# Optimization experiments

Hardware: AMD Instinct MI355X
Metric: run time of the kernel (lower is better)

## Reference

```python
import jax, jax.numpy as jnp
import numpy as np

N_IN = 64
N_HID = 128


def setup_inputs() -> dict:
    key = jax.random.key(0)
    k_x, k_wih, k_bih, k_whh, k_bhh = jax.random.split(key, 5)
    S, B = 1024, 4096
    x = jax.random.normal(k_x, (S, B, N_IN), dtype=jnp.float32)
    # torch.nn.Linear weights: W [out, in], b [out]
    lim_ih = 1.0 / np.sqrt(N_IN)
    lim_hh = 1.0 / np.sqrt(N_HID)
    W_ih = jax.random.uniform(k_wih, (N_HID, N_IN), jnp.float32, -lim_ih, lim_ih)
    b_ih = jax.random.uniform(k_bih, (N_HID,), jnp.float32, -lim_ih, lim_ih)
    W_hh = jax.random.uniform(k_whh, (N_HID, N_HID), jnp.float32, -lim_hh, lim_hh)
    b_hh = jax.random.uniform(k_bhh, (N_HID,), jnp.float32, -lim_hh, lim_hh)
    return {"x": x, "W_ih": W_ih, "b_ih": b_ih, "W_hh": W_hh, "b_hh": b_hh}


def reference(x, W_ih, b_ih, W_hh, b_hh):
    # Elman RNN: h_t = tanh(x_t @ W_ih^T + b_ih + h_{t-1} @ W_hh^T + b_hh)
    # x: [S, B, 64]; returns final hidden state [B, 128]
    B = x.shape[1]
    h0 = jnp.zeros((B, N_HID), dtype=x.dtype)
    # Precompute the input projection for all timesteps (one big GEMM).
    xp = jnp.einsum('sbi,hi->sbh', x, W_ih) + b_ih  # [S, B, 128]

    def step(h, xp_t):
        h_new = jnp.tanh(xp_t + h @ W_hh.T + b_hh)
        return h_new, None

    h_final, _ = jax.lax.scan(step, h0, xp)
    return h_final
```

## Files before the change

kernel.cpp:

```cpp
#include <hip/hip_runtime.h>

#define S_LEN 1024
#define BATCH 4096
#define NIN 64
#define NHID 128
#define BT 16

typedef __attribute__((ext_vector_type(8))) short bf16x8;
typedef __attribute__((ext_vector_type(4))) float f32x4;

__device__ __forceinline__ unsigned cvt_pk(float lo, float hi) {
    unsigned r;
    asm("v_cvt_pk_bf16_f32 %0, %1, %2" : "=v"(r) : "v"(lo), "v"(hi));
    return r;
}
__device__ __forceinline__ float tanh_fast(float z) {
    float u = __builtin_amdgcn_exp2f(z * 2.885390081777927f);
    return (u - 1.0f) * __builtin_amdgcn_rcpf(u + 1.0f);
}
__device__ __forceinline__ void lds_barrier() {
    asm volatile("s_waitcnt lgkmcnt(0)\n\ts_barrier" ::: "memory");
    __builtin_amdgcn_sched_barrier(0);
}

#define MFMA __builtin_amdgcn_mfma_f32_16x16x32_bf16


__global__ __launch_bounds__(256, 1)
void rnn_kernel(const float* __restrict__ x,
                const float* __restrict__ W_ih,
                const float* __restrict__ b_ih,
                const float* __restrict__ W_hh,
                const float* __restrict__ b_hh,
                float* __restrict__ out)
{
    __shared__ __align__(16) char lds[8192];
    const int tid  = threadIdx.x;
    const int wv   = tid >> 6;
    const int lane = tid & 63;
    const int col  = lane & 15;
    const int kg   = lane >> 4;
    const int bb0  = blockIdx.x * BT;

    for (int i = tid; i < 2048; i += 256) ((int*)lds)[i] = 0;

    const int OWN = wv;
    char* lbx = lds + (lane << 4);
    char*       wp  = lbx + (OWN << 10);
    const char* rp1 = lbx + ((((OWN + 1) & 3)) << 10);
    const char* rp2 = lbx + ((((OWN + 2) & 3)) << 10);
    const char* rp3 = lbx + ((((OWN + 3) & 3)) << 10);

    bf16x8 whh0[4], whh1[4];
    const int tt0 = 2 * OWN, tt1 = tt0 + 1;
    #pragma unroll
    for (int q = 0; q < 4; ++q) {
        const int kkq = (OWN + q) & 3;
        {
            const float* pw = W_hh + (16 * tt0 + col) * NHID + 32 * kkq + 4 * kg;
            f32x4 c0 = *(const f32x4*)(pw);
            f32x4 c1 = *(const f32x4*)(pw + 16);
            union { bf16x8 v; unsigned u[4]; } fr;
            fr.u[0] = cvt_pk(c0[0], c0[1]); fr.u[1] = cvt_pk(c0[2], c0[3]);
            fr.u[2] = cvt_pk(c1[0], c1[1]); fr.u[3] = cvt_pk(c1[2], c1[3]);
            whh0[q] = fr.v;
        }
        {
            const float* pw = W_hh + (16 * tt1 + col) * NHID + 32 * kkq + 4 * kg;
            f32x4 c0 = *(const f32x4*)(pw);
            f32x4 c1 = *(const f32x4*)(pw + 16);
            union { bf16x8 v; unsigned u[4]; } fr;
            fr.u[0] = cvt_pk(c0[0], c0[1]); fr.u[1] = cvt_pk(c0[2], c0[3]);
            fr.u[2] = cvt_pk(c1[0], c1[1]); fr.u[3] = cvt_pk(c1[2], c1[3]);
            whh1[q] = fr.v;
        }
    }
    bf16x8 wihA0, wihB0, wihA1, wihB1;
    {
        const float* q0 = W_ih + (16 * tt0 + col) * NIN + 8 * kg;
        const float* q1 = W_ih + (16 * tt1 + col) * NIN + 8 * kg;
        union { bf16x8 v; unsigned u[4]; } fr;
        f32x4 c0, c1;
        c0 = *(const f32x4*)(q0);      c1 = *(const f32x4*)(q0 + 4);
        fr.u[0] = cvt_pk(c0[0], c0[1]); fr.u[1] = cvt_pk(c0[2], c0[3]);
        fr.u[2] = cvt_pk(c1[0], c1[1]); fr.u[3] = cvt_pk(c1[2], c1[3]);
        wihA0 = fr.v;
        c0 = *(const f32x4*)(q0 + 32); c1 = *(const f32x4*)(q0 + 36);
        fr.u[0] = cvt_pk(c0[0], c0[1]); fr.u[1] = cvt_pk(c0[2], c0[3]);
        fr.u[2] = cvt_pk(c1[0], c1[1]); fr.u[3] = cvt_pk(c1[2], c1[3]);
        wihB0 = fr.v;
        c0 = *(const f32x4*)(q1);      c1 = *(const f32x4*)(q1 + 4);
        fr.u[0] = cvt_pk(c0[0], c0[1]); fr.u[1] = cvt_pk(c0[2], c0[3]);
        fr.u[2] = cvt_pk(c1[0], c1[1]); fr.u[3] = cvt_pk(c1[2], c1[3]);
        wihA1 = fr.v;
        c0 = *(const f32x4*)(q1 + 32); c1 = *(const f32x4*)(q1 + 36);
        fr.u[0] = cvt_pk(c0[0], c0[1]); fr.u[1] = cvt_pk(c0[2], c0[3]);
        fr.u[2] = cvt_pk(c1[0], c1[1]); fr.u[3] = cvt_pk(c1[2], c1[3]);
        wihB1 = fr.v;
    }
    f32x4 bias0, bias1;
    {
        f32x4 bi = *(const f32x4*)(b_ih + 16 * tt0 + 4 * kg);
        f32x4 bh = *(const f32x4*)(b_hh + 16 * tt0 + 4 * kg);
        bias0 = bi + bh;
        bi = *(const f32x4*)(b_ih + 16 * tt1 + 4 * kg);
        bh = *(const f32x4*)(b_hh + 16 * tt1 + 4 * kg);
        bias1 = bi + bh;
    }

    const float* xlane = x + ((size_t)bb0 + col) * NIN + kg * 8;

    auto loadStage = [&](f32x4& v0, f32x4& v1, f32x4& v2, f32x4& v3, int t) {
        if (t < S_LEN) {
            const float* p = xlane + (size_t)t * (BATCH * NIN);
            v0 = *(const f32x4*)(p);      v1 = *(const f32x4*)(p + 4);
            v2 = *(const f32x4*)(p + 32); v3 = *(const f32x4*)(p + 36);
        }
    };
    auto computeXP = [&](const f32x4& v0, const f32x4& v1,
                         const f32x4& v2, const f32x4& v3,
                         f32x4& o0, f32x4& o1) {
        union { bf16x8 v; unsigned u[4]; } xa, xb;
        xa.u[0] = cvt_pk(v0[0], v0[1]); xa.u[1] = cvt_pk(v0[2], v0[3]);
        xa.u[2] = cvt_pk(v1[0], v1[1]); xa.u[3] = cvt_pk(v1[2], v1[3]);
        xb.u[0] = cvt_pk(v2[0], v2[1]); xb.u[1] = cvt_pk(v2[2], v2[3]);
        xb.u[2] = cvt_pk(v3[0], v3[1]); xb.u[3] = cvt_pk(v3[2], v3[3]);
        f32x4 p0 = bias0, p1 = bias1;
        p0 = MFMA(wihA0, xa.v, p0, 0, 0, 0);
        p1 = MFMA(wihA1, xa.v, p1, 0, 0, 0);
        p0 = MFMA(wihB0, xb.v, p0, 0, 0, 0);
        p1 = MFMA(wihB1, xb.v, p1, 0, 0, 0);
        o0 = p0; o1 = p1;
    };

    f32x4 S00, S01, S02, S03, S10, S11, S12, S13;
    f32x4 S20, S21, S22, S23, S30, S31, S32, S33;
    loadStage(S00, S01, S02, S03, 0);
    loadStage(S10, S11, S12, S13, 1);
    loadStage(S20, S21, S22, S23, 2);
    loadStage(S30, S31, S32, S33, 3);
    f32x4 xc0, xc1, xn0, xn1;
    computeXP(S00, S01, S02, S03, xc0, xc1);
    loadStage(S00, S01, S02, S03, 4);
    bf16x8 Bo = {0, 0, 0, 0, 0, 0, 0, 0};
    __syncthreads();

    auto cstep = [&](int t, f32x4& s0, f32x4& s1, f32x4& s2, f32x4& s3,
                     const f32x4& c0, const f32x4& c1,
                     f32x4& n0, f32x4& n1, bool last) {
        const int rb = (t & 1) << 12;
        bf16x8 P1 = *(const bf16x8*)(rp1 + rb);
        bf16x8 P2 = *(const bf16x8*)(rp2 + rb);
        bf16x8 P3 = *(const bf16x8*)(rp3 + rb);

        f32x4 a0 = c0, a1 = c1;
        a0 = MFMA(whh0[0], Bo, a0, 0, 0, 0);
        a1 = MFMA(whh1[0], Bo, a1, 0, 0, 0);

        computeXP(s0, s1, s2, s3, n0, n1);
        loadStage(s0, s1, s2, s3, t + 5);

        a0 = MFMA(whh0[1], P1, a0, 0, 0, 0);
        a1 = MFMA(whh1[1], P1, a1, 0, 0, 0);
        a0 = MFMA(whh0[2], P2, a0, 0, 0, 0);
        a1 = MFMA(whh1[2], P2, a1, 0, 0, 0);
        a0 = MFMA(whh0[3], P3, a0, 0, 0, 0);
        a1 = MFMA(whh1[3], P3, a1, 0, 0, 0);

        #pragma unroll
        for (int i = 0; i < 4; ++i) a0[i] = tanh_fast(a0[i]);
        #pragma unroll
        for (int i = 0; i < 4; ++i) a1[i] = tanh_fast(a1[i]);

        if (last) {
            float* ob = out + ((size_t)bb0 + col) * NHID + 32 * OWN + 4 * kg;
            *(f32x4*)(ob)      = a0;
            *(f32x4*)(ob + 16) = a1;
        } else {
            union { bf16x8 v; unsigned u[4]; } fb;
            fb.u[0] = cvt_pk(a0[0], a0[1]); fb.u[1] = cvt_pk(a0[2], a0[3]);
            fb.u[2] = cvt_pk(a1[0], a1[1]); fb.u[3] = cvt_pk(a1[2], a1[3]);
            Bo = fb.v;
            *(bf16x8*)(wp + (((t + 1) & 1) << 12)) = Bo;
        }
        lds_barrier();
    };

    for (int m = 0; m < 255; ++m) {
        const int t = 4 * m;
        cstep(t + 0, S10, S11, S12, S13, xc0, xc1, xn0, xn1, false);
        cstep(t + 1, S20, S21, S22, S23, xn0, xn1, xc0, xc1, false);
        cstep(t + 2, S30, S31, S32, S33, xc0, xc1, xn0, xn1, false);
        cstep(t + 3, S00, S01, S02, S03, xn0, xn1, xc0, xc1, false);
    }
    cstep(1020, S10, S11, S12, S13, xc0, xc1, xn0, xn1, false);
    cstep(1021, S20, S21, S22, S23, xn0, xn1, xc0, xc1, false);
    cstep(1022, S30, S31, S32, S33, xc0, xc1, xn0, xn1, false);
    cstep(1023, S00, S01, S02, S03, xn0, xn1, xc0, xc1, true);
}

extern "C" void kernel_launch(void* const* d_in, const int* in_sizes, int n_in,
                              void* d_out, int out_size, void* d_ws, size_t ws_size,
                              hipStream_t stream) {
    const float* x    = (const float*)d_in[0];
    const float* W_ih = (const float*)d_in[1];
    const float* b_ih = (const float*)d_in[2];
    const float* W_hh = (const float*)d_in[3];
    const float* b_hh = (const float*)d_in[4];
    float* out = (float*)d_out;

    dim3 grid(BATCH / BT);
    dim3 block(256);
    rnn_kernel<<<grid, block, 0, stream>>>(x, W_ih, b_ih, W_hh, b_hh, out);
}
```

Measured before the change: 455.5 us.

## Exchange partial W_hh products through LDS instead of hidden-state fragments

Restructures the recurrent step so each wave multiplies its own hidden slice by every output tile's W_hh block and writes fp32 partial sums to LDS. After the barrier, the owner wave sums the partials and applies tanh, which takes the MFMA chain off the critical path between barriers. The cost is eight times more LDS traffic (64 KB buffer, 6 float4 writes and reads per step) and a shallower x prefetch. tanh is also rewritten as 1 - 2/(u+1).

New measurement: 548.9 us. 20.5% more time.

```diff
diff --git a/kernel.cpp b/kernel.cpp
--- a/kernel.cpp
+++ b/kernel.cpp
@@ -16,7 +16,7 @@
 }
 __device__ __forceinline__ float tanh_fast(float z) {
     float u = __builtin_amdgcn_exp2f(z * 2.885390081777927f);
-    return (u - 1.0f) * __builtin_amdgcn_rcpf(u + 1.0f);
+    return fmaf(-2.0f, __builtin_amdgcn_rcpf(u + 1.0f), 1.0f);
 }
 __device__ __forceinline__ void lds_barrier() {
     asm volatile("s_waitcnt lgkmcnt(0)\n\ts_barrier" ::: "memory");
@@ -24,6 +24,13 @@
 }
 
 #define MFMA __builtin_amdgcn_mfma_f32_16x16x32_bf16
+
+__device__ __forceinline__ bf16x8 pack8(const f32x4& a, const f32x4& b) {
+    union { bf16x8 v; unsigned u[4]; } r;
+    r.u[0] = cvt_pk(a[0], a[1]); r.u[1] = cvt_pk(a[2], a[3]);
+    r.u[2] = cvt_pk(b[0], b[1]); r.u[3] = cvt_pk(b[2], b[3]);
+    return r.v;
+}
 
 
 __global__ __launch_bounds__(256, 1)
@@ -34,7 +41,7 @@
                 const float* __restrict__ b_hh,
                 float* __restrict__ out)
 {
-    __shared__ __align__(16) char lds[8192];
+    __shared__ __align__(16) char lds[65536];
     const int tid  = threadIdx.x;
     const int wv   = tid >> 6;
     const int lane = tid & 63;
@@ -42,61 +49,44 @@
     const int kg   = lane >> 4;
     const int bb0  = blockIdx.x * BT;
 
-    for (int i = tid; i < 2048; i += 256) ((int*)lds)[i] = 0;
+    for (int i = tid; i < 16384; i += 256) ((int*)lds)[i] = 0;
 
     const int OWN = wv;
+    const int o1 = (OWN + 1) & 3, o2 = (OWN + 2) & 3, o3 = (OWN + 3) & 3;
     char* lbx = lds + (lane << 4);
-    char*       wp  = lbx + (OWN << 10);
-    const char* rp1 = lbx + ((((OWN + 1) & 3)) << 10);
-    const char* rp2 = lbx + ((((OWN + 2) & 3)) << 10);
-    const char* rp3 = lbx + ((((OWN + 3) & 3)) << 10);
-
-    bf16x8 whh0[4], whh1[4];
+    char* w10 = lbx + ((o1 * 8 + OWN * 2 + 0) << 10);
+    char* w11 = lbx + ((o1 * 8 + OWN * 2 + 1) << 10);
+    char* w20 = lbx + ((o2 * 8 + OWN * 2 + 0) << 10);
+    char* w21 = lbx + ((o2 * 8 + OWN * 2 + 1) << 10);
+    char* w30 = lbx + ((o3 * 8 + OWN * 2 + 0) << 10);
+    char* w31 = lbx + ((o3 * 8 + OWN * 2 + 1) << 10);
+    const char* r10 = lbx + ((OWN * 8 + o1 * 2 + 0) << 10);
+    const char* r11 = lbx + ((OWN * 8 + o1 * 2 + 1) << 10);
+    const char* r20 = lbx + ((OWN * 8 + o2 * 2 + 0) << 10);
+    const char* r21 = lbx + ((OWN * 8 + o2 * 2 + 1) << 10);
+    const char* r30 = lbx + ((OWN * 8 + o3 * 2 + 0) << 10);
+    const char* r31 = lbx + ((OWN * 8 + o3 * 2 + 1) << 10);
+
+    auto loadWhh = [&](int nt) -> bf16x8 {
+        const float* pw = W_hh + (size_t)(16 * nt + col) * NHID + 32 * OWN + 4 * kg;
+        f32x4 c0 = *(const f32x4*)(pw);
+        f32x4 c1 = *(const f32x4*)(pw + 16);
+        return pack8(c0, c1);
+    };
+    bf16x8 whhP10 = loadWhh(2 * o1),  whhP11 = loadWhh(2 * o1 + 1);
+    bf16x8 whhP20 = loadWhh(2 * o2),  whhP21 = loadWhh(2 * o2 + 1);
+    bf16x8 whhP30 = loadWhh(2 * o3),  whhP31 = loadWhh(2 * o3 + 1);
+    bf16x8 whhO0  = loadWhh(2 * OWN), whhO1  = loadWhh(2 * OWN + 1);
+
     const int tt0 = 2 * OWN, tt1 = tt0 + 1;
-    #pragma unroll
-    for (int q = 0; q < 4; ++q) {
-        const int kkq = (OWN + q) & 3;
-        {
-            const float* pw = W_hh + (16 * tt0 + col) * NHID + 32 * kkq + 4 * kg;
-            f32x4 c0 = *(const f32x4*)(pw);
-            f32x4 c1 = *(const f32x4*)(pw + 16);
-            union { bf16x8 v; unsigned u[4]; } fr;
-            fr.u[0] = cvt_pk(c0[0], c0[1]); fr.u[1] = cvt_pk(c0[2], c0[3]);
-            fr.u[2] = cvt_pk(c1[0], c1[1]); fr.u[3] = cvt_pk(c1[2], c1[3]);
-            whh0[q] = fr.v;
-        }
-        {
-            const float* pw = W_hh + (16 * tt1 + col) * NHID + 32 * kkq + 4 * kg;
-            f32x4 c0 = *(const f32x4*)(pw);
-            f32x4 c1 = *(const f32x4*)(pw + 16);
-            union { bf16x8 v; unsigned u[4]; } fr;
-            fr.u[0] = cvt_pk(c0[0], c0[1]); fr.u[1] = cvt_pk(c0[2], c0[3]);
-            fr.u[2] = cvt_pk(c1[0], c1[1]); fr.u[3] = cvt_pk(c1[2], c1[3]);
-            whh1[q] = fr.v;
-        }
-    }
     bf16x8 wihA0, wihB0, wihA1, wihB1;
     {
-        const float* q0 = W_ih + (16 * tt0 + col) * NIN + 8 * kg;
-        const float* q1 = W_ih + (16 * tt1 + col) * NIN + 8 * kg;
-        union { bf16x8 v; unsigned u[4]; } fr;
-        f32x4 c0, c1;
-        c0 = *(const f32x4*)(q0);      c1 = *(const f32x4*)(q0 + 4);
-        fr.u[0] = cvt_pk(c0[0], c0[1]); fr.u[1] = cvt_pk(c0[2], c0[3]);
-        fr.u[2] = cvt_pk(c1[0], c1[1]); fr.u[3] = cvt_pk(c1[2], c1[3]);
-        wihA0 = fr.v;
-        c0 = *(const f32x4*)(q0 + 32); c1 = *(const f32x4*)(q0 + 36);
-        fr.u[0] = cvt_pk(c0[0], c0[1]); fr.u[1] = cvt_pk(c0[2], c0[3]);
-        fr.u[2] = cvt_pk(c1[0], c1[1]); fr.u[3] = cvt_pk(c1[2], c1[3]);
-        wihB0 = fr.v;
-        c0 = *(const f32x4*)(q1);      c1 = *(const f32x4*)(q1 + 4);
-        fr.u[0] = cvt_pk(c0[0], c0[1]); fr.u[1] = cvt_pk(c0[2], c0[3]);
-        fr.u[2] = cvt_pk(c1[0], c1[1]); fr.u[3] = cvt_pk(c1[2], c1[3]);
-        wihA1 = fr.v;
-        c0 = *(const f32x4*)(q1 + 32); c1 = *(const f32x4*)(q1 + 36);
-        fr.u[0] = cvt_pk(c0[0], c0[1]); fr.u[1] = cvt_pk(c0[2], c0[3]);
-        fr.u[2] = cvt_pk(c1[0], c1[1]); fr.u[3] = cvt_pk(c1[2], c1[3]);
-        wihB1 = fr.v;
+        const float* q0 = W_ih + (size_t)(16 * tt0 + col) * NIN + 8 * kg;
+        const float* q1 = W_ih + (size_t)(16 * tt1 + col) * NIN + 8 * kg;
+        wihA0 = pack8(*(const f32x4*)(q0),      *(const f32x4*)(q0 + 4));
+        wihB0 = pack8(*(const f32x4*)(q0 + 32), *(const f32x4*)(q0 + 36));
+        wihA1 = pack8(*(const f32x4*)(q1),      *(const f32x4*)(q1 + 4));
+        wihB1 = pack8(*(const f32x4*)(q1 + 32), *(const f32x4*)(q1 + 36));
     }
     f32x4 bias0, bias1;
     {
@@ -109,7 +99,6 @@
     }
 
     const float* xlane = x + ((size_t)bb0 + col) * NIN + kg * 8;
-
     auto loadStage = [&](f32x4& v0, f32x4& v1, f32x4& v2, f32x4& v3, int t) {
         if (t < S_LEN) {
             const float* p = xlane + (size_t)t * (BATCH * NIN);
@@ -117,86 +106,90 @@
             v2 = *(const f32x4*)(p + 32); v3 = *(const f32x4*)(p + 36);
         }
     };
-    auto computeXP = [&](const f32x4& v0, const f32x4& v1,
-                         const f32x4& v2, const f32x4& v3,
-                         f32x4& o0, f32x4& o1) {
-        union { bf16x8 v; unsigned u[4]; } xa, xb;
-        xa.u[0] = cvt_pk(v0[0], v0[1]); xa.u[1] = cvt_pk(v0[2], v0[3]);
-        xa.u[2] = cvt_pk(v1[0], v1[1]); xa.u[3] = cvt_pk(v1[2], v1[3]);
-        xb.u[0] = cvt_pk(v2[0], v2[1]); xb.u[1] = cvt_pk(v2[2], v2[3]);
-        xb.u[2] = cvt_pk(v3[0], v3[1]); xb.u[3] = cvt_pk(v3[2], v3[3]);
+    auto computeXP = [&](const bf16x8& xa, const bf16x8& xb,
+                         f32x4& q0, f32x4& q1) {
         f32x4 p0 = bias0, p1 = bias1;
-        p0 = MFMA(wihA0, xa.v, p0, 0, 0, 0);
-        p1 = MFMA(wihA1, xa.v, p1, 0, 0, 0);
-        p0 = MFMA(wihB0, xb.v, p0, 0, 0, 0);
-        p1 = MFMA(wihB1, xb.v, p1, 0, 0, 0);
-        o0 = p0; o1 = p1;
-    };
-
-    f32x4 S00, S01, S02, S03, S10, S11, S12, S13;
-    f32x4 S20, S21, S22, S23, S30, S31, S32, S33;
-    loadStage(S00, S01, S02, S03, 0);
-    loadStage(S10, S11, S12, S13, 1);
-    loadStage(S20, S21, S22, S23, 2);
-    loadStage(S30, S31, S32, S33, 3);
-    f32x4 xc0, xc1, xn0, xn1;
-    computeXP(S00, S01, S02, S03, xc0, xc1);
-    loadStage(S00, S01, S02, S03, 4);
-    bf16x8 Bo = {0, 0, 0, 0, 0, 0, 0, 0};
+        p0 = MFMA(wihA0, xa, p0, 0, 0, 0);
+        p1 = MFMA(wihA1, xa, p1, 0, 0, 0);
+        p0 = MFMA(wihB0, xb, p0, 0, 0, 0);
+        p1 = MFMA(wihB1, xb, p1, 0, 0, 0);
+        q0 = p0; q1 = p1;
+    };
+
+    f32x4 A0, A1, A2, A3, B0, B1, B2, B3;
+    bf16x8 PCa, PCb, PNa, PNb;
+    f32x4 pO0, pO1;
+    loadStage(A0, A1, A2, A3, 0);
+    PCa = pack8(A0, A1); PCb = pack8(A2, A3);
+    computeXP(PCa, PCb, pO0, pO1);
+    loadStage(A0, A1, A2, A3, 1);
+    PCa = pack8(A0, A1); PCb = pack8(A2, A3);
+    loadStage(A0, A1, A2, A3, 2);
+    loadStage(B0, B1, B2, B3, 3);
     __syncthreads();
 
     auto cstep = [&](int t, f32x4& s0, f32x4& s1, f32x4& s2, f32x4& s3,
-                     const f32x4& c0, const f32x4& c1,
-                     f32x4& n0, f32x4& n1, bool last) {
-        const int rb = (t & 1) << 12;
-        bf16x8 P1 = *(const bf16x8*)(rp1 + rb);
-        bf16x8 P2 = *(const bf16x8*)(rp2 + rb);
-        bf16x8 P3 = *(const bf16x8*)(rp3 + rb);
-
-        f32x4 a0 = c0, a1 = c1;
-        a0 = MFMA(whh0[0], Bo, a0, 0, 0, 0);
-        a1 = MFMA(whh1[0], Bo, a1, 0, 0, 0);
-
-        computeXP(s0, s1, s2, s3, n0, n1);
-        loadStage(s0, s1, s2, s3, t + 5);
-
-        a0 = MFMA(whh0[1], P1, a0, 0, 0, 0);
-        a1 = MFMA(whh1[1], P1, a1, 0, 0, 0);
-        a0 = MFMA(whh0[2], P2, a0, 0, 0, 0);
-        a1 = MFMA(whh1[2], P2, a1, 0, 0, 0);
-        a0 = MFMA(whh0[3], P3, a0, 0, 0, 0);
-        a1 = MFMA(whh1[3], P3, a1, 0, 0, 0);
-
+                     const bf16x8& pca, const bf16x8& pcb,
+                     bf16x8& pna, bf16x8& pnb, bool last) {
+        const int rb = (t & 1) << 15;
+        f32x4 q10 = *(const f32x4*)(r10 + rb);
+        f32x4 q11 = *(const f32x4*)(r11 + rb);
+        f32x4 q20 = *(const f32x4*)(r20 + rb);
+        f32x4 q21 = *(const f32x4*)(r21 + rb);
+        f32x4 q30 = *(const f32x4*)(r30 + rb);
+        f32x4 q31 = *(const f32x4*)(r31 + rb);
+        f32x4 xq0, xq1;
+        if (t + 1 < S_LEN) computeXP(pca, pcb, xq0, xq1);
+        f32x4 pre0 = (pO0 + q10) + (q20 + q30);
+        f32x4 pre1 = (pO1 + q11) + (q21 + q31);
+        f32x4 v0, v1;
         #pragma unroll
-        for (int i = 0; i < 4; ++i) a0[i] = tanh_fast(a0[i]);
+        for (int i = 0; i < 4; ++i) v0[i] = tanh_fast(pre0[i]);
         #pragma unroll
-        for (int i = 0; i < 4; ++i) a1[i] = tanh_fast(a1[i]);
+        for (int i = 0; i < 4; ++i) v1[i] = tanh_fast(pre1[i]);
 
         if (last) {
             float* ob = out + ((size_t)bb0 + col) * NHID + 32 * OWN + 4 * kg;
-            *(f32x4*)(ob)      = a0;
-            *(f32x4*)(ob + 16) = a1;
-        } else {
+            *(f32x4*)(ob)      = v0;
+            *(f32x4*)(ob + 16) = v1;
+            lds_barrier();
+            return;
+        }
+        bf16x8 Bo;
+        {
             union { bf16x8 v; unsigned u[4]; } fb;
-            fb.u[0] = cvt_pk(a0[0], a0[1]); fb.u[1] = cvt_pk(a0[2], a0[3]);
-            fb.u[2] = cvt_pk(a1[0], a1[1]); fb.u[3] = cvt_pk(a1[2], a1[3]);
+            fb.u[0] = cvt_pk(v0[0], v0[1]); fb.u[1] = cvt_pk(v0[2], v0[3]);
+            fb.u[2] = cvt_pk(v1[0], v1[1]); fb.u[3] = cvt_pk(v1[2], v1[3]);
             Bo = fb.v;
-            *(bf16x8*)(wp + (((t + 1) & 1) << 12)) = Bo;
         }
+        const int nb = ((t + 1) & 1) << 15;
+        const f32x4 z4 = {0.f, 0.f, 0.f, 0.f};
+        f32x4 g10 = MFMA(whhP10, Bo, z4, 0, 0, 0);
+        f32x4 g11 = MFMA(whhP11, Bo, z4, 0, 0, 0);
+        f32x4 g20 = MFMA(whhP20, Bo, z4, 0, 0, 0);
+        f32x4 g21 = MFMA(whhP21, Bo, z4, 0, 0, 0);
+        f32x4 g30 = MFMA(whhP30, Bo, z4, 0, 0, 0);
+        f32x4 g31 = MFMA(whhP31, Bo, z4, 0, 0, 0);
+        *(f32x4*)(w10 + nb) = g10;
+        *(f32x4*)(w11 + nb) = g11;
+        *(f32x4*)(w20 + nb) = g20;
+        *(f32x4*)(w21 + nb) = g21;
+        *(f32x4*)(w30 + nb) = g30;
+        *(f32x4*)(w31 + nb) = g31;
+        pO0 = MFMA(whhO0, Bo, xq0, 0, 0, 0);
+        pO1 = MFMA(whhO1, Bo, xq1, 0, 0, 0);
+        if (t + 2 < S_LEN) { pna = pack8(s0, s1); pnb = pack8(s2, s3); }
+        loadStage(s0, s1, s2, s3, t + 4);
         lds_barrier();
     };
 
-    for (int m = 0; m < 255; ++m) {
-        const int t = 4 * m;
-        cstep(t + 0, S10, S11, S12, S13, xc0, xc1, xn0, xn1, false);
-        cstep(t + 1, S20, S21, S22, S23, xn0, xn1, xc0, xc1, false);
-        cstep(t + 2, S30, S31, S32, S33, xc0, xc1, xn0, xn1, false);
-        cstep(t + 3, S00, S01, S02, S03, xn0, xn1, xc0, xc1, false);
+    for (int m = 0; m < 511; ++m) {
+        const int t = 2 * m;
+        cstep(t,     A0, A1, A2, A3, PCa, PCb, PNa, PNb, false);
+        cstep(t + 1, B0, B1, B2, B3, PNa, PNb, PCa, PCb, false);
     }
-    cstep(1020, S10, S11, S12, S13, xc0, xc1, xn0, xn1, false);
-    cstep(1021, S20, S21, S22, S23, xn0, xn1, xc0, xc1, false);
-    cstep(1022, S30, S31, S32, S33, xc0, xc1, xn0, xn1, false);
-    cstep(1023, S00, S01, S02, S03, xn0, xn1, xc0, xc1, true);
+    cstep(1022, A0, A1, A2, A3, PCa, PCb, PNa, PNb, false);
+    cstep(1023, B0, B1, B2, B3, PNa, PNb, PCa, PCb, true);
 }
 
 extern "C" void kernel_launch(void* const* d_in, const int* in_sizes, int n_in,
```

## Split hidden dimension across eight waves per block, one 16-row tile each

Applied to the files above, without the earlier changes.

Each block now runs 8 waves instead of 4, and each wave owns a single 16-column slice of the hidden state rather than two. Per step a wave does 4 recurrent MFMAs split into two independent accumulator chains, then writes a half-width bf16 fragment to the shared LDS hidden buffer. This shortens the serial per-step critical path per wave at the cost of double the barrier participants and redundant x loads across waves. The tanh is also rewritten as 1 - 2/(u+1) to save an instruction.

New measurement: 893.4 us. +96.1%, slower.

```diff
diff --git a/kernel.cpp b/kernel.cpp
--- a/kernel.cpp
+++ b/kernel.cpp
@@ -16,7 +16,7 @@
 }
 __device__ __forceinline__ float tanh_fast(float z) {
     float u = __builtin_amdgcn_exp2f(z * 2.885390081777927f);
-    return (u - 1.0f) * __builtin_amdgcn_rcpf(u + 1.0f);
+    return fmaf(-2.0f, __builtin_amdgcn_rcpf(u + 1.0f), 1.0f);
 }
 __device__ __forceinline__ void lds_barrier() {
     asm volatile("s_waitcnt lgkmcnt(0)\n\ts_barrier" ::: "memory");
@@ -25,8 +25,15 @@
 
 #define MFMA __builtin_amdgcn_mfma_f32_16x16x32_bf16
 
+__device__ __forceinline__ bf16x8 pack8(const f32x4& a, const f32x4& b) {
+    union { bf16x8 v; unsigned u[4]; } r;
+    r.u[0] = cvt_pk(a[0], a[1]); r.u[1] = cvt_pk(a[2], a[3]);
+    r.u[2] = cvt_pk(b[0], b[1]); r.u[3] = cvt_pk(b[2], b[3]);
+    return r.v;
+}
 
-__global__ __launch_bounds__(256, 1)
+
+__global__ __launch_bounds__(512, 2)
 void rnn_kernel(const float* __restrict__ x,
                 const float* __restrict__ W_ih,
                 const float* __restrict__ b_ih,
@@ -42,74 +49,43 @@
     const int kg   = lane >> 4;
     const int bb0  = blockIdx.x * BT;
 
-    for (int i = tid; i < 2048; i += 256) ((int*)lds)[i] = 0;
+    for (int i = tid; i < 2048; i += 512) ((int*)lds)[i] = 0;
 
     const int OWN = wv;
     char* lbx = lds + (lane << 4);
-    char*       wp  = lbx + (OWN << 10);
-    const char* rp1 = lbx + ((((OWN + 1) & 3)) << 10);
-    const char* rp2 = lbx + ((((OWN + 2) & 3)) << 10);
-    const char* rp3 = lbx + ((((OWN + 3) & 3)) << 10);
+    char* wp  = lbx + ((OWN >> 1) << 10) + ((OWN & 1) << 3);
+    const char* rp0 = lbx;
+    const char* rp1 = lbx + (1 << 10);
+    const char* rp2 = lbx + (2 << 10);
+    const char* rp3 = lbx + (3 << 10);
 
-    bf16x8 whh0[4], whh1[4];
-    const int tt0 = 2 * OWN, tt1 = tt0 + 1;
-    #pragma unroll
-    for (int q = 0; q < 4; ++q) {
-        const int kkq = (OWN + q) & 3;
-        {
-            const float* pw = W_hh + (16 * tt0 + col) * NHID + 32 * kkq + 4 * kg;
+    bf16x8 whh0, whh1, whh2, whh3;
+    {
+        const float* rowp = W_hh + (size_t)(16 * OWN + col) * NHID + 4 * kg;
+        #pragma unroll
+        for (int q = 0; q < 4; ++q) {
+            const float* pw = rowp + 32 * q;
             f32x4 c0 = *(const f32x4*)(pw);
             f32x4 c1 = *(const f32x4*)(pw + 16);
-            union { bf16x8 v; unsigned u[4]; } fr;
-            fr.u[0] = cvt_pk(c0[0], c0[1]); fr.u[1] = cvt_pk(c0[2], c0[3]);
-            fr.u[2] = cvt_pk(c1[0], c1[1]); fr.u[3] = cvt_pk(c1[2], c1[3]);
-            whh0[q] = fr.v;
-        }
-        {
-            const float* pw = W_hh + (16 * tt1 + col) * NHID + 32 * kkq + 4 * kg;
-            f32x4 c0 = *(const f32x4*)(pw);
-            f32x4 c1 = *(const f32x4*)(pw + 16);
-            union { bf16x8 v; unsigned u[4]; } fr;
-            fr.u[0] = cvt_pk(c0[0], c0[1]); fr.u[1] = cvt_pk(c0[2], c0[3]);
-            fr.u[2] = cvt_pk(c1[0], c1[1]); fr.u[3] = cvt_pk(c1[2], c1[3]);
-            whh1[q] = fr.v;
+            bf16x8 fr = pack8(c0, c1);
+            if (q == 0) whh0 = fr; else if (q == 1) whh1 = fr;
+            else if (q == 2) whh2 = fr; else whh3 = fr;
         }
     }
-    bf16x8 wihA0, wihB0, wihA1, wihB1;
+    bf16x8 wihA, wihB;
     {
-        const float* q0 = W_ih + (16 * tt0 + col) * NIN + 8 * kg;
-        const float* q1 = W_ih + (16 * tt1 + col) * NIN + 8 * kg;
-        union { bf16x8 v; unsigned u[4]; } fr;
-        f32x4 c0, c1;
-        c0 = *(const f32x4*)(q0);      c1 = *(const f32x4*)(q0 + 4);
-        fr.u[0] = cvt_pk(c0[0], c0[1]); fr.u[1] = cvt_pk(c0[2], c0[3]);
-        fr.u[2] = cvt_pk(c1[0], c1[1]); fr.u[3] = cvt_pk(c1[2], c1[3]);
-        wihA0 = fr.v;
-        c0 = *(const f32x4*)(q0 + 32); c1 = *(const f32x4*)(q0 + 36);
-        fr.u[0] = cvt_pk(c0[0], c0[1]); fr.u[1] = cvt_pk(c0[2], c0[3]);
-        fr.u[2] = cvt_pk(c1[0], c1[1]); fr.u[3] = cvt_pk(c1[2], c1[3]);
-        wihB0 = fr.v;
-        c0 = *(const f32x4*)(q1);      c1 = *(const f32x4*)(q1 + 4);
-        fr.u[0] = cvt_pk(c0[0], c0[1]); fr.u[1] = cvt_pk(c0[2], c0[3]);
-        fr.u[2] = cvt_pk(c1[0], c1[1]); fr.u[3] = cvt_pk(c1[2], c1[3]);
-        wihA1 = fr.v;
-        c0 = *(const f32x4*)(q1 + 32); c1 = *(const f32x4*)(q1 + 36);
-        fr.u[0] = cvt_pk(c0[0], c0[1]); fr.u[1] = cvt_pk(c0[2], c0[3]);
-        fr.u[2] = cvt_pk(c1[0], c1[1]); fr.u[3] = cvt_pk(c1[2], c1[3]);
-        wihB1 = fr.v;
+        const float* q0 = W_ih + (size_t)(16 * OWN + col) * NIN + 8 * kg;
+        wihA = pack8(*(const f32x4*)(q0),      *(const f32x4*)(q0 + 4));
+        wihB = pack8(*(const f32x4*)(q0 + 32), *(const f32x4*)(q0 + 36));
     }
-    f32x4 bias0, bias1;
+    f32x4 biasv;
     {
-        f32x4 bi = *(const f32x4*)(b_ih + 16 * tt0 + 4 * kg);
-        f32x4 bh = *(const f32x4*)(b_hh + 16 * tt0 + 4 * kg);
-        bias0 = bi + bh;
-        bi = *(const f32x4*)(b_ih + 16 * tt1 + 4 * kg);
-        bh = *(const f32x4*)(b_hh + 16 * tt1 + 4 * kg);
-        bias1 = bi + bh;
+        f32x4 bi = *(const f32x4*)(b_ih + 16 * OWN + 4 * kg);
+        f32x4 bh = *(const f32x4*)(b_hh + 16 * OWN + 4 * kg);
+        biasv = bi + bh;
     }
 
     const float* xlane = x + ((size_t)bb0 + col) * NIN + kg * 8;
-
     auto loadStage = [&](f32x4& v0, f32x4& v1, f32x4& v2, f32x4& v3, int t) {
         if (t < S_LEN) {
             const float* p = xlane + (size_t)t * (BATCH * NIN);
@@ -118,19 +94,16 @@
         }
     };
     auto computeXP = [&](const f32x4& v0, const f32x4& v1,
-                         const f32x4& v2, const f32x4& v3,
-                         f32x4& o0, f32x4& o1) {
+                         const f32x4& v2, const f32x4& v3, f32x4& o0) {
         union { bf16x8 v; unsigned u[4]; } xa, xb;
         xa.u[0] = cvt_pk(v0[0], v0[1]); xa.u[1] = cvt_pk(v0[2], v0[3]);
         xa.u[2] = cvt_pk(v1[0], v1[1]); xa.u[3] = cvt_pk(v1[2], v1[3]);
         xb.u[0] = cvt_pk(v2[0], v2[1]); xb.u[1] = cvt_pk(v2[2], v2[3]);
         xb.u[2] = cvt_pk(v3[0], v3[1]); xb.u[3] = cvt_pk(v3[2], v3[3]);
-        f32x4 p0 = bias0, p1 = bias1;
-        p0 = MFMA(wihA0, xa.v, p0, 0, 0, 0);
-        p1 = MFMA(wihA1, xa.v, p1, 0, 0, 0);
-        p0 = MFMA(wihB0, xb.v, p0, 0, 0, 0);
-        p1 = MFMA(wihB1, xb.v, p1, 0, 0, 0);
-        o0 = p0; o1 = p1;
+        f32x4 p0 = biasv;
+        p0 = MFMA(wihA, xa.v, p0, 0, 0, 0);
+        p0 = MFMA(wihB, xb.v, p0, 0, 0, 0);
+        o0 = p0;
     };
 
     f32x4 S00, S01, S02, S03, S10, S11, S12, S13;
@@ -139,64 +112,57 @@
     loadStage(S10, S11, S12, S13, 1);
     loadStage(S20, S21, S22, S23, 2);
     loadStage(S30, S31, S32, S33, 3);
-    f32x4 xc0, xc1, xn0, xn1;
-    computeXP(S00, S01, S02, S03, xc0, xc1);
+    f32x4 xc, xn;
+    computeXP(S00, S01, S02, S03, xc);
     loadStage(S00, S01, S02, S03, 4);
-    bf16x8 Bo = {0, 0, 0, 0, 0, 0, 0, 0};
     __syncthreads();
 
     auto cstep = [&](int t, f32x4& s0, f32x4& s1, f32x4& s2, f32x4& s3,
-                     const f32x4& c0, const f32x4& c1,
-                     f32x4& n0, f32x4& n1, bool last) {
+                     const f32x4& c, f32x4& n, bool last) {
         const int rb = (t & 1) << 12;
-        bf16x8 P1 = *(const bf16x8*)(rp1 + rb);
-        bf16x8 P2 = *(const bf16x8*)(rp2 + rb);
-        bf16x8 P3 = *(const bf16x8*)(rp3 + rb);
+        bf16x8 B0 = *(const bf16x8*)(rp0 + rb);
+        bf16x8 B1 = *(const bf16x8*)(rp1 + rb);
+        bf16x8 B2 = *(const bf16x8*)(rp2 + rb);
+        bf16x8 B3 = *(const bf16x8*)(rp3 + rb);
 
-        f32x4 a0 = c0, a1 = c1;
-        a0 = MFMA(whh0[0], Bo, a0, 0, 0, 0);
-        a1 = MFMA(whh1[0], Bo, a1, 0, 0, 0);
-
-        computeXP(s0, s1, s2, s3, n0, n1);
+        computeXP(s0, s1, s2, s3, n);
         loadStage(s0, s1, s2, s3, t + 5);
 
-        a0 = MFMA(whh0[1], P1, a0, 0, 0, 0);
-        a1 = MFMA(whh1[1], P1, a1, 0, 0, 0);
-        a0 = MFMA(whh0[2], P2, a0, 0, 0, 0);
-        a1 = MFMA(whh1[2], P2, a1, 0, 0, 0);
-        a0 = MFMA(whh0[3], P3, a0, 0, 0, 0);
-        a1 = MFMA(whh1[3], P3, a1, 0, 0, 0);
+        f32x4 c0 = c;
+        const f32x4 z4 = {0.f, 0.f, 0.f, 0.f};
+        f32x4 c1 = z4;
+        c0 = MFMA(whh0, B0, c0, 0, 0, 0);
+        c1 = MFMA(whh2, B2, c1, 0, 0, 0);
+        c0 = MFMA(whh1, B1, c0, 0, 0, 0);
+        c1 = MFMA(whh3, B3, c1, 0, 0, 0);
+        f32x4 pre = c0 + c1;
 
+        f32x4 v;
         #pragma unroll
-        for (int i = 0; i < 4; ++i) a0[i] = tanh_fast(a0[i]);
-        #pragma unroll
-        for (int i = 0; i < 4; ++i) a1[i] = tanh_fast(a1[i]);
+        for (int i = 0; i < 4; ++i) v[i] = tanh_fast(pre[i]);
 
         if (last) {
-            float* ob = out + ((size_t)bb0 + col) * NHID + 32 * OWN + 4 * kg;
-            *(f32x4*)(ob)      = a0;
-            *(f32x4*)(ob + 16) = a1;
+            *(f32x4*)(out + ((size_t)bb0 + col) * NHID + 16 * OWN + 4 * kg) = v;
         } else {
-            union { bf16x8 v; unsigned u[4]; } fb;
-            fb.u[0] = cvt_pk(a0[0], a0[1]); fb.u[1] = cvt_pk(a0[2], a0[3]);
-            fb.u[2] = cvt_pk(a1[0], a1[1]); fb.u[3] = cvt_pk(a1[2], a1[3]);
-            Bo = fb.v;
-            *(bf16x8*)(wp + (((t + 1) & 1) << 12)) = Bo;
+            uint2 hb;
+            hb.x = cvt_pk(v[0], v[1]);
+            hb.y = cvt_pk(v[2], v[3]);
+            *(uint2*)(wp + (((t + 1) & 1) << 12)) = hb;
         }
         lds_barrier();
     };
 
     for (int m = 0; m < 255; ++m) {
         const int t = 4 * m;
-        cstep(t + 0, S10, S11, S12, S13, xc0, xc1, xn0, xn1, false);
-        cstep(t + 1, S20, S21, S22, S23, xn0, xn1, xc0, xc1, false);
-        cstep(t + 2, S30, S31, S32, S33, xc0, xc1, xn0, xn1, false);
-        cstep(t + 3, S00, S01, S02, S03, xn0, xn1, xc0, xc1, false);
+        cstep(t + 0, S10, S11, S12, S13, xc, xn, false);
+        cstep(t + 1, S20, S21, S22, S23, xn, xc, false);
+        cstep(t + 2, S30, S31, S32, S33, xc, xn, false);
+        cstep(t + 3, S00, S01, S02, S03, xn, xc, false);
     }
-    cstep(1020, S10, S11, S12, S13, xc0, xc1, xn0, xn1, false);
-    cstep(1021, S20, S21, S22, S23, xn0, xn1, xc0, xc1, false);
-    cstep(1022, S30, S31, S32, S33, xc0, xc1, xn0, xn1, false);
-    cstep(1023, S00, S01, S02, S03, xn0, xn1, xc0, xc1, true);
+    cstep(1020, S10, S11, S12, S13, xc, xn, false);
+    cstep(1021, S20, S21, S22, S23, xn, xc, false);
+    cstep(1022, S30, S31, S32, S33, xc, xn, false);
+    cstep(1023, S00, S01, S02, S03, xn, xc, true);
 }
 
 extern "C" void kernel_launch(void* const* d_in, const int* in_sizes, int n_in,
@@ -210,6 +176,6 @@
     float* out = (float*)d_out;
 
     dim3 grid(BATCH / BT);
-    dim3 block(256);
+    dim3 block(512);
     rnn_kernel<<<grid, block, 0, stream>>>(x, W_ih, b_ih, W_hh, b_hh, out);
 }
```
